# Optimization experiments

Hardware: AMD Instinct MI355X
Metric: run time of the kernel (lower is better)

## Reference

```python
import jax, jax.numpy as jnp
import numpy as np

R = 16            # search_range
D = 2 * R + 1     # 33 offsets per axis -> 1089 cost channels
B, C, H, W = 64, 256, 16, 16
OUT = 512         # conv channels for search_range=16
FULLY = 1024
EPS_BN = 1e-5
EPS_NORM = 1e-12
LRELU_SLOPE = 0.01


def l2_normalize(x):
    # torch F.normalize(x, dim=1, p=2): x / clamp_min(||x||_2, 1e-12)
    n = jnp.sqrt(jnp.sum(x * x, axis=1, keepdims=True))
    return x / jnp.maximum(n, EPS_NORM)


def cost_volume(c1, warp, r):
    # Fused equivalent of the original (2r+1)^2 Python-loop of slice/mul/mean:
    # one dense correlation GEMM over the padded map, then a gather of the
    # diagonal-band entries. cost[b,dy,dx,i,j] = mean_c c1[b,c,i,j]*pad[b,c,i+dy,j+dx]
    b, c, h, w = c1.shape
    d = 2 * r + 1
    padded = jnp.pad(warp, ((0, 0), (0, 0), (r, r), (r, r)))          # (B,C,h+2r,w+2r)
    full = jnp.einsum('bcij,bcuv->bijuv', c1, padded) / c             # (B,h,w,h+2r,w+2r)
    dy = jnp.arange(d)
    ii = jnp.arange(h)
    jj = jnp.arange(w)
    I = ii[None, None, :, None]                 # (1,1,h,1)
    J = jj[None, None, None, :]                 # (1,1,1,w)
    U = dy[:, None, None, None] + I             # (d,1,h,1)
    V = dy[None, :, None, None] + J             # (1,d,1,w)
    cost = full[:, I, J, U, V]                  # (B,d,d,h,w)
    cost = cost.reshape(b, d * d, h, w)
    return jnp.where(cost > 0, cost, LRELU_SLOPE * cost)  # LeakyReLU(0.01)


def conv_bn_relu(x, Wc, bc, g, be, stride):
    y = jax.lax.conv_general_dilated(
        x, Wc, window_strides=(stride, stride), padding=((1, 1), (1, 1)),
        dimension_numbers=('NCHW', 'OIHW', 'NCHW'))
    y = y + bc[None, :, None, None]
    # training-mode BatchNorm: biased batch stats over (B,H,W)
    mu = jnp.mean(y, axis=(0, 2, 3), keepdims=True)
    var = jnp.var(y, axis=(0, 2, 3), keepdims=True)
    y = (y - mu) * jax.lax.rsqrt(var + EPS_BN)
    y = y * g[None, :, None, None] + be[None, :, None, None]
    return jnp.maximum(y, 0.0)


def setup_inputs() -> dict:
    key = jax.random.key(0)
    ks = jax.random.split(key, 10)
    s = 0.02
    inp = {
        'feature1': jax.random.normal(ks[0], (B, C, H, W), jnp.float32),
        'feature2': jax.random.normal(ks[1], (B, C, H, W), jnp.float32),
        'W1': jax.random.normal(ks[2], (OUT, D * D, 3, 3), jnp.float32) * s,
        'b1': jnp.zeros((OUT,), jnp.float32),
        'g1': jnp.ones((OUT,), jnp.float32),
        'be1': jnp.zeros((OUT,), jnp.float32),
        'W2': jax.random.normal(ks[3], (OUT, OUT, 3, 3), jnp.float32) * s,
        'b2': jnp.zeros((OUT,), jnp.float32),
        'g2': jnp.ones((OUT,), jnp.float32),
        'be2': jnp.zeros((OUT,), jnp.float32),
        'W3': jax.random.normal(ks[4], (OUT, OUT, 3, 3), jnp.float32) * s,
        'b3': jnp.zeros((OUT,), jnp.float32),
        'g3': jnp.ones((OUT,), jnp.float32),
        'be3': jnp.zeros((OUT,), jnp.float32),
        'Wf1': jax.random.normal(ks[5], (FULLY, 256 * OUT), jnp.float32) * s,
        'bf1': jnp.zeros((FULLY,), jnp.float32),
        'Wf2': jax.random.normal(ks[6], (8, FULLY), jnp.float32) * s,
        'bf2': jnp.zeros((8,), jnp.float32),
    }
    return inp


def reference(feature1, feature2, W1, b1, g1, be1, W2, b2, g2, be2,
              W3, b3, g3, be3, Wf1, bf1, Wf2, bf2):
    # warped=False: normalize both feature maps
    gc = cost_volume(l2_normalize(feature1), l2_normalize(feature2), R)
    x = conv_bn_relu(gc, W1, b1, g1, be1, 1)
    x = conv_bn_relu(x, W2, b2, g2, be2, 1)
    x = conv_bn_relu(x, W3, b3, g3, be3, 1)
    x = x.reshape(x.shape[0], -1)               # (B, 512*16*16)
    x = jnp.maximum(x @ Wf1.T + bf1, 0.0)       # Linear + ReLU
    # Dropout treated as identity (deterministic reference)
    offset = x @ Wf2.T + bf2                    # (B, 8)
    return offset
```

## Files before the change

### kernel.cpp

```cpp
#include <hip/hip_runtime.h>
#include <hip/hip_bf16.h>
#include <stdint.h>


typedef unsigned short ushort_t;
typedef __attribute__((ext_vector_type(8))) short     bf16x8;
typedef __attribute__((ext_vector_type(8))) unsigned short u16x8;
typedef __attribute__((ext_vector_type(2))) unsigned short u16x2;
typedef __attribute__((ext_vector_type(4))) float     f32x4;

#define NB   64
#define NC   256
#define NP   256
#define KP1  1152
#define NOUT 512
#define NROWS 16384
#define KFC  131072
#define NF   1024
#define KSPL 32

__device__ __forceinline__ unsigned short f2bf(float x) {
  union { float f; unsigned u; } c; c.f = x;
  unsigned r = c.u + 0x7FFFu + ((c.u >> 16) & 1u);
  return (unsigned short)(r >> 16);
}
__device__ __forceinline__ float b2f(unsigned short u) {
  union { unsigned u; float f; } c; c.u = ((unsigned)u) << 16; return c.f;
}

__device__ __forceinline__ void gl_lds16(const void* g, void* l) {
  __builtin_amdgcn_global_load_lds(
      (const __attribute__((address_space(1))) unsigned int*)g,
      (__attribute__((address_space(3))) unsigned int*)l, 16, 0, 0);
}

__device__ __forceinline__ f32x4 mfma16(bf16x8 a, bf16x8 b, f32x4 c) {
  return __builtin_amdgcn_mfma_f32_16x16x32_bf16(a, b, c, 0, 0, 0);
}

__global__ __launch_bounds__(1024) void l2norm_t(
    const float* __restrict__ f1, const float* __restrict__ f2,
    ushort_t* __restrict__ AT, ushort_t* __restrict__ N2T)
{
  __shared__ float red[4][256];
  const float* src = blockIdx.y ? f2 : f1;
  ushort_t*    dst = blockIdx.y ? N2T : AT;
  const int b = blockIdx.x;
  const int pos = threadIdx.x & 255, q = threadIdx.x >> 8;
  const float* sb = src + (size_t)b * NC * NP;
  float v[64];
#pragma unroll
  for (int k = 0; k < 64; ++k) v[k] = sb[(q * 64 + k) * NP + pos];
  float sq = 0.f;
#pragma unroll
  for (int k = 0; k < 64; ++k) sq += v[k] * v[k];
  red[q][pos] = sq;
  __syncthreads();
  float tot = red[0][pos] + red[1][pos] + red[2][pos] + red[3][pos];
  float sc = 1.f / fmaxf(sqrtf(tot), 1e-12f);
  ushort_t* db = dst + ((size_t)b * NP + pos) * NC;
#pragma unroll
  for (int j = 0; j < 8; ++j) {
    u16x8 pk;
#pragma unroll
    for (int k = 0; k < 8; ++k) pk[k] = f2bf(v[j * 8 + k] * sc);
    *(u16x8*)(db + q * 64 + j * 8) = pk;
  }
}

#define T1P (9 * NOUT * KP1)
#define T23 (9 * NOUT * 512)
__global__ __launch_bounds__(256) void pack_all(
    const float* __restrict__ W1, const float* __restrict__ W2,
    const float* __restrict__ W3, ushort_t* __restrict__ Wp1,
    ushort_t* __restrict__ Wp2, ushort_t* __restrict__ Wp3)
{
  int p = blockIdx.x * 256 + threadIdx.x;
  const float* W; ushort_t* Wp; int Cin, Kp, q;
  if (p < T1P)            { W = W1; Wp = Wp1; Cin = 1089; Kp = KP1; q = p; }
  else if (p < T1P + T23) { W = W2; Wp = Wp2; Cin = 512;  Kp = 512; q = p - T1P; }
  else if (p < T1P + 2 * T23) { W = W3; Wp = Wp3; Cin = 512; Kp = 512; q = p - T1P - T23; }
  else return;
  int tap = q / (NOUT * Kp);
  int rem = q - tap * (NOUT * Kp);
  int o   = rem / Kp;
  int cin = rem - o * Kp;
  float v = (cin < Cin) ? W[((size_t)o * Cin + cin) * 9 + tap] : 0.f;
  Wp[q] = f2bf(v);
}

__global__ __launch_bounds__(256) void corr_gemm(
    const ushort_t* __restrict__ AT,
    const ushort_t* __restrict__ N2T,
    float* __restrict__ C)
{
  __shared__ ushort_t As[128 * 64];
  __shared__ ushort_t Bs[128 * 64];
  const int tid = threadIdx.x, lane = tid & 63, wave = tid >> 6;
  const int wr = wave >> 1, wc = wave & 1;
  const int la = lane & 15, lb = lane >> 4;
  const int b  = blockIdx.z;
  const int m0 = blockIdx.y * 128;
  const int n0 = blockIdx.x * 128;

  f32x4 acc[4][4];
#pragma unroll
  for (int i = 0; i < 4; ++i)
#pragma unroll
    for (int j = 0; j < 4; ++j) acc[i][j] = (f32x4){0.f, 0.f, 0.f, 0.f};

  const ushort_t* srcA[4];
  const ushort_t* srcB[4];
#pragma unroll
  for (int s = 0; s < 4; ++s) {
    int idx = tid + (s << 8);
    int row = idx >> 3, c16 = idx & 7;
    srcA[s] = AT  + ((size_t)b * NP + m0 + row) * NC + c16 * 8;
    srcB[s] = N2T + ((size_t)b * NP + n0 + row) * NC + c16 * 8;
  }

  for (int kc = 0; kc < NC; kc += 64) {
#pragma unroll
    for (int s = 0; s < 4; ++s) {
      int idx = tid + (s << 8);
      gl_lds16(srcA[s] + kc, &As[idx * 8]);
      gl_lds16(srcB[s] + kc, &Bs[idx * 8]);
    }
    __syncthreads();
#pragma unroll
    for (int kk = 0; kk < 2; ++kk) {
      bf16x8 af[4], bfv[4];
#pragma unroll
      for (int mi = 0; mi < 4; ++mi)
        af[mi] = *(const bf16x8*)&As[(wr * 64 + mi * 16 + la) * 64 + kk * 32 + lb * 8];
#pragma unroll
      for (int ni = 0; ni < 4; ++ni)
        bfv[ni] = *(const bf16x8*)&Bs[(wc * 64 + ni * 16 + la) * 64 + kk * 32 + lb * 8];
#pragma unroll
      for (int mi = 0; mi < 4; ++mi)
#pragma unroll
        for (int ni = 0; ni < 4; ++ni)
          acc[mi][ni] = mfma16(af[mi], bfv[ni], acc[mi][ni]);
    }
    __syncthreads();
  }

#pragma unroll
  for (int ni = 0; ni < 4; ++ni) {
    int col = n0 + wc * 64 + ni * 16 + la;
#pragma unroll
    for (int mi = 0; mi < 4; ++mi) {
      int p = m0 + wr * 64 + mi * 16 + lb * 4;
#pragma unroll
      for (int r = 0; r < 4; ++r)
        C[((size_t)b * NP + p + r) * NP + col] = acc[mi][ni][r];
    }
  }
}

__global__ __launch_bounds__(576) void cost_write(
    const float* __restrict__ C, ushort_t* __restrict__ costT)
{
  __shared__ float row[256];
  const int ij = blockIdx.x, b = blockIdx.y, tid = threadIdx.x;
  const float* cr = C + ((size_t)b * NP + ij) * NP;
  if (tid < 256) row[tid] = cr[tid];
  __syncthreads();
  const int i = ij >> 4, j = ij & 15;
  const int d0 = tid * 2;
  u16x2 pk;
#pragma unroll
  for (int q = 0; q < 2; ++q) {
    int dd = d0 + q;
    int dy = dd / 33;
    int dx = dd - dy * 33;
    int oi = dy + i - 16, oj = dx + j - 16;
    float v = 0.f;
    if (((unsigned)oi < 16u) & ((unsigned)oj < 16u))
      v = row[oi * 16 + oj] * (1.f / 256.f);
    v = v > 0.f ? v : 0.01f * v;
    pk[q] = f2bf(v);
  }
  *(u16x2*)(costT + ((size_t)b * NP + ij) * KP1 + d0) = pk;
}

__global__ __launch_bounds__(512, 1) void conv_fused(
    const ushort_t* __restrict__ X, const ushort_t* __restrict__ Wp,
    const float* __restrict__ bias, ushort_t* __restrict__ Y,
    float* __restrict__ st, const int K, const int TPT, const int NT,
    const ushort_t* __restrict__ zerot)
{
  __shared__ ushort_t lds[2 * 24576];
  const int tid = threadIdx.x;
  const int lane = tid & 63, wave = tid >> 6;
  const int wr = wave >> 2, wc = wave & 3;
  const int la = lane & 15, lb = lane >> 4;

  const int bid = blockIdx.x;
  const int L = ((bid & 7) << 5) + (bid >> 3);
  const int b = L >> 2;
  const int n0 = (L & 3) << 7;

  int amask[4];
  const ushort_t* abase[4];
  const ushort_t* bbase[2];
#pragma unroll
  for (int s = 0; s < 4; ++s) {
    int idx = tid + (s << 9);
    int ks = idx & 7, loc = (idx >> 3) & 63;
    int rA = ((s & 1) << 7) + ((s >> 1) << 6) + loc;
    int i = rA >> 4, j = rA & 15;
    int m = 0;
#pragma unroll
    for (int tap = 0; tap < 9; ++tap) {
      int i2 = i + tap / 3 - 1, j2 = j + tap % 3 - 1;
      if (((unsigned)i2 < 16u) & ((unsigned)j2 < 16u)) m |= 1 << tap;
    }
    amask[s] = m;
    abase[s] = X + (size_t)(b * NP + rA) * K + ((ks ^ (rA & 7)) << 3);
  }
#pragma unroll
  for (int s = 0; s < 2; ++s) {
    int idx = tid + (s << 9);
    int ks = idx & 7, loc = (idx >> 3) & 63;
    int rB = (s << 6) + loc;
    bbase[s] = Wp + (size_t)(n0 + rB) * K + ((ks ^ (rB & 7)) << 3);
  }

  const int ck0 = ((0 + lb) ^ (la & 7)) << 3;
  const int ck1 = ((4 + lb) ^ (la & 7)) << 3;
  const int a_base = wr * 4096 + la * 64;
  const int b_off  = 16384 + (wc * 32 + la) * 64;

  f32x4 acc[8][2];
#pragma unroll
  for (int i = 0; i < 8; ++i)
#pragma unroll
    for (int j = 0; j < 2; ++j) acc[i][j] = (f32x4){0.f, 0.f, 0.f, 0.f};

  auto tile_par = [&](int tg, int& toffA, size_t& wtap, int& tap) {
    tap = tg / TPT;
    int kc = (tg - tap * TPT) << 6;
    int ty = tap / 3;
    toffA = (ty * 16 + (tap - 3 * ty) - 17) * K + kc;
    wtap  = (size_t)tap * NOUT * K + kc;
  };

#define FSTAGE_A(S) { const ushort_t* gp = ((amask[S] >> tapN) & 1) ? abase[S] + toffN : zerot; \
                      gl_lds16(gp, &bufn[(tid + ((S) << 9)) * 8]); }
#define FSTAGE_B(S) gl_lds16(bbase[S] + wtapN, &bufn[16384 + (tid + ((S) << 9)) * 8]);
#define FREAD_A03() \
  Af[0][0] = *(const bf16x8*)&buf[a_base + 0    + ck0]; Af[0][1] = *(const bf16x8*)&buf[a_base + 0    + ck1]; \
  Af[1][0] = *(const bf16x8*)&buf[a_base + 1024 + ck0]; Af[1][1] = *(const bf16x8*)&buf[a_base + 1024 + ck1]; \
  Af[2][0] = *(const bf16x8*)&buf[a_base + 2048 + ck0]; Af[2][1] = *(const bf16x8*)&buf[a_base + 2048 + ck1]; \
  Af[3][0] = *(const bf16x8*)&buf[a_base + 3072 + ck0]; Af[3][1] = *(const bf16x8*)&buf[a_base + 3072 + ck1];
#define FREAD_A47() \
  Af[0][0] = *(const bf16x8*)&buf[a_base + 8192 + 0    + ck0]; Af[0][1] = *(const bf16x8*)&buf[a_base + 8192 + 0    + ck1]; \
  Af[1][0] = *(const bf16x8*)&buf[a_base + 8192 + 1024 + ck0]; Af[1][1] = *(const bf16x8*)&buf[a_base + 8192 + 1024 + ck1]; \
  Af[2][0] = *(const bf16x8*)&buf[a_base + 8192 + 2048 + ck0]; Af[2][1] = *(const bf16x8*)&buf[a_base + 8192 + 2048 + ck1]; \
  Af[3][0] = *(const bf16x8*)&buf[a_base + 8192 + 3072 + ck0]; Af[3][1] = *(const bf16x8*)&buf[a_base + 8192 + 3072 + ck1];
#define FREAD_B() \
  Bf[0][0] = *(const bf16x8*)&buf[b_off + 0    + ck0]; Bf[0][1] = *(const bf16x8*)&buf[b_off + 0    + ck1]; \
  Bf[1][0] = *(const bf16x8*)&buf[b_off + 1024 + ck0]; Bf[1][1] = *(const bf16x8*)&buf[b_off + 1024 + ck1];
#define FMFMA(AB) \
  acc[(AB)+0][0] = mfma16(Af[0][0], Bf[0][0], acc[(AB)+0][0]); \
  acc[(AB)+0][1] = mfma16(Af[0][0], Bf[1][0], acc[(AB)+0][1]); \
  acc[(AB)+1][0] = mfma16(Af[1][0], Bf[0][0], acc[(AB)+1][0]); \
  acc[(AB)+1][1] = mfma16(Af[1][0], Bf[1][0], acc[(AB)+1][1]); \
  acc[(AB)+2][0] = mfma16(Af[2][0], Bf[0][0], acc[(AB)+2][0]); \
  acc[(AB)+2][1] = mfma16(Af[2][0], Bf[1][0], acc[(AB)+2][1]); \
  acc[(AB)+3][0] = mfma16(Af[3][0], Bf[0][0], acc[(AB)+3][0]); \
  acc[(AB)+3][1] = mfma16(Af[3][0], Bf[1][0], acc[(AB)+3][1]); \
  acc[(AB)+0][0] = mfma16(Af[0][1], Bf[0][1], acc[(AB)+0][0]); \
  acc[(AB)+0][1] = mfma16(Af[0][1], Bf[1][1], acc[(AB)+0][1]); \
  acc[(AB)+1][0] = mfma16(Af[1][1], Bf[0][1], acc[(AB)+1][0]); \
  acc[(AB)+1][1] = mfma16(Af[1][1], Bf[1][1], acc[(AB)+1][1]); \
  acc[(AB)+2][0] = mfma16(Af[2][1], Bf[0][1], acc[(AB)+2][0]); \
  acc[(AB)+2][1] = mfma16(Af[2][1], Bf[1][1], acc[(AB)+2][1]); \
  acc[(AB)+3][0] = mfma16(Af[3][1], Bf[0][1], acc[(AB)+3][0]); \
  acc[(AB)+3][1] = mfma16(Af[3][1], Bf[1][1], acc[(AB)+3][1]);

  {
    ushort_t* bufn = &lds[0];
    int tapN, toffN; size_t wtapN;
    tile_par(0, toffN, wtapN, tapN);
    FSTAGE_A(0) FSTAGE_A(1) FSTAGE_B(0) FSTAGE_B(1) FSTAGE_A(2) FSTAGE_A(3)
  }
  asm volatile("s_waitcnt vmcnt(2)" ::: "memory");
  __builtin_amdgcn_s_barrier();

  for (int t = 0; t < NT - 1; ++t) {
    const ushort_t* buf = &lds[(t & 1) * 24576];
    ushort_t* bufn = &lds[((t + 1) & 1) * 24576];
    int tapN, toffN; size_t wtapN;
    tile_par(t + 1, toffN, wtapN, tapN);
    bf16x8 Af[4][2], Bf[2][2];

    FREAD_A03()
    FREAD_B()
    FSTAGE_A(0) FSTAGE_A(1) FSTAGE_B(0) FSTAGE_B(1)
    asm volatile("s_waitcnt vmcnt(4)" ::: "memory");
    __builtin_amdgcn_s_barrier();
    asm volatile("s_waitcnt lgkmcnt(0)" ::: "memory");
    __builtin_amdgcn_sched_barrier(0);
    __builtin_amdgcn_s_setprio(1);
    FMFMA(0)
    __builtin_amdgcn_s_setprio(0);

    FREAD_A47()
    FSTAGE_A(2) FSTAGE_A(3)
    asm volatile("s_waitcnt vmcnt(2)" ::: "memory");
    __builtin_amdgcn_s_barrier();
    asm volatile("s_waitcnt lgkmcnt(0)" ::: "memory");
    __builtin_amdgcn_sched_barrier(0);
    __builtin_amdgcn_s_setprio(1);
    FMFMA(4)
    __builtin_amdgcn_s_setprio(0);
  }

  {
    const ushort_t* buf = &lds[((NT - 1) & 1) * 24576];
    bf16x8 Af[4][2], Bf[2][2];
    FREAD_A03()
    FREAD_B()
    asm volatile("s_waitcnt vmcnt(0)" ::: "memory");
    __builtin_amdgcn_s_barrier();
    asm volatile("s_waitcnt lgkmcnt(0)" ::: "memory");
    __builtin_amdgcn_sched_barrier(0);
    FMFMA(0)
    FREAD_A47()
    asm volatile("s_waitcnt lgkmcnt(0)" ::: "memory");
    __builtin_amdgcn_sched_barrier(0);
    FMFMA(4)
  }

#pragma unroll
  for (int ni = 0; ni < 2; ++ni) {
    int col = n0 + wc * 32 + ni * 16 + la;
    float bv = bias[col];
    float s = 0.f, qq = 0.f;
#pragma unroll
    for (int mi = 0; mi < 8; ++mi) {
      int row = b * NP + wr * 128 + mi * 16 + lb * 4;
#pragma unroll
      for (int r = 0; r < 4; ++r) {
        float v = acc[mi][ni][r] + bv;
        Y[(size_t)(row + r) * NOUT + col] = f2bf(v);
        s += v; qq += v * v;
      }
    }
    s  += __shfl_xor(s, 16);  s  += __shfl_xor(s, 32);
    qq += __shfl_xor(qq, 16); qq += __shfl_xor(qq, 32);
    if (lb == 0) {
      atomicAdd(&st[col], s);
      atomicAdd(&st[512 + col], qq);
    }
  }
#undef FSTAGE_A
#undef FSTAGE_B
#undef FREAD_A03
#undef FREAD_A47
#undef FREAD_B
#undef FMFMA
}

__global__ __launch_bounds__(256) void bn_apply_s(
    const ushort_t* __restrict__ Y, const float* __restrict__ st,
    const float* __restrict__ g, const float* __restrict__ be,
    ushort_t* __restrict__ Xo)
{
  const size_t idx = (size_t)blockIdx.x * 256 + threadIdx.x;
  u16x8 a = *(const u16x8*)(Y + idx * 8);
  const int c0 = (int)((idx * 8) & 511);
  u16x8 pk;
#pragma unroll
  for (int q = 0; q < 8; ++q) {
    int cc = c0 + q;
    float y = b2f(a[q]);
    float mu  = st[cc] * (1.f / 16384.f);
    float var = st[512 + cc] * (1.f / 16384.f) - mu * mu;
    float s = rsqrtf(var + 1e-5f) * g[cc];
    pk[q] = f2bf(fmaxf((y - mu) * s + be[cc], 0.f));
  }
  *(u16x8*)(Xo + idx * 8) = pk;
}

__global__ __launch_bounds__(256) void bn_apply_ts(
    const ushort_t* __restrict__ Y, const float* __restrict__ st,
    const float* __restrict__ g, const float* __restrict__ be,
    ushort_t* __restrict__ Xf)
{
  __shared__ ushort_t T[64][65];
  const int c0  = blockIdx.x * 64;
  const int ij0 = blockIdx.y * 64;
  const int b   = blockIdx.z;
  const int tid = threadIdx.x;

#pragma unroll
  for (int it = 0; it < 16; ++it) {
    int e = it * 256 + tid;
    int ij = e >> 6, c = e & 63;
    int cg = c0 + c;
    float y = b2f(Y[((size_t)(b * NP + ij0 + ij)) * NOUT + cg]);
    float mu  = st[cg] * (1.f / 16384.f);
    float var = st[512 + cg] * (1.f / 16384.f) - mu * mu;
    float s = rsqrtf(var + 1e-5f) * g[cg];
    T[ij][c] = f2bf(fmaxf((y - mu) * s + be[cg], 0.f));
  }
  __syncthreads();
#pragma unroll
  for (int it = 0; it < 16; ++it) {
    int e = it * 256 + tid;
    int cr = e >> 6, ijc = e & 63;
    Xf[(size_t)b * KFC + (size_t)(c0 + cr) * NP + ij0 + ijc] = T[ijc][cr];
  }
}

__device__ __forceinline__ u16x8 pack8(float4 a, float4 b) {
  u16x8 r;
  r[0] = f2bf(a.x); r[1] = f2bf(a.y); r[2] = f2bf(a.z); r[3] = f2bf(a.w);
  r[4] = f2bf(b.x); r[5] = f2bf(b.y); r[6] = f2bf(b.z); r[7] = f2bf(b.w);
  return r;
}

__global__ __launch_bounds__(256) void fc1_gemm(
    const ushort_t* __restrict__ Xf, const float* __restrict__ Wf1,
    float* __restrict__ hacc)
{
  __shared__ ushort_t As[2][4096];
  __shared__ ushort_t Bs[2][4096];
  const int tid = threadIdx.x, lane = tid & 63, wave = tid >> 6;
  const int la = lane & 15, lb = lane >> 4;
  const int f0 = blockIdx.x * 64;
  const int k0 = blockIdx.y * 4096;

  f32x4 acc[4];
#pragma unroll
  for (int i = 0; i < 4; ++i) acc[i] = (f32x4){0.f, 0.f, 0.f, 0.f};

  const ushort_t* xrow0 = Xf + (size_t)(tid >> 3) * KFC + k0 + (tid & 7) * 8;
  const ushort_t* xrow1 = Xf + (size_t)((tid + 256) >> 3) * KFC + k0 + (tid & 7) * 8;
  const int brow = tid >> 2, kseg = (tid & 3) * 16;
  const float* wrow = Wf1 + (size_t)(f0 + brow) * KFC + k0 + kseg;
  const int bwr = brow * 64 + kseg;

  float4 w0, w1, w2, w3;

  gl_lds16(xrow0, &As[0][tid * 8]);
  gl_lds16(xrow1, &As[0][(tid + 256) * 8]);
  w0 = *(const float4*)(wrow + 0);
  w1 = *(const float4*)(wrow + 4);
  w2 = *(const float4*)(wrow + 8);
  w3 = *(const float4*)(wrow + 12);
  *(u16x8*)&Bs[0][bwr]     = pack8(w0, w1);
  *(u16x8*)&Bs[0][bwr + 8] = pack8(w2, w3);
  gl_lds16(xrow0 + 64, &As[1][tid * 8]);
  gl_lds16(xrow1 + 64, &As[1][(tid + 256) * 8]);
  w0 = *(const float4*)(wrow + 64);
  w1 = *(const float4*)(wrow + 68);
  w2 = *(const float4*)(wrow + 72);
  w3 = *(const float4*)(wrow + 76);
  asm volatile("s_waitcnt lgkmcnt(0)" ::: "memory");
  __builtin_amdgcn_s_barrier();

#define FC1_MFMA(CUR) \
  { \
    _Pragma("unroll") \
    for (int kk = 0; kk < 2; ++kk) { \
      bf16x8 bfv = *(const bf16x8*)&Bs[CUR][(wave * 16 + la) * 64 + kk * 32 + lb * 8]; \
      _Pragma("unroll") \
      for (int mi = 0; mi < 4; ++mi) { \
        bf16x8 av = *(const bf16x8*)&As[CUR][(mi * 16 + la) * 64 + kk * 32 + lb * 8]; \
        acc[mi] = mfma16(av, bfv, acc[mi]); \
      } \
    } \
  }

  for (int t = 0; t < 62; ++t) {
    const int cur = t & 1, nxt = cur ^ 1;
    FC1_MFMA(cur)
    *(u16x8*)&Bs[nxt][bwr]     = pack8(w0, w1);
    *(u16x8*)&Bs[nxt][bwr + 8] = pack8(w2, w3);
    {
      const float* wp = wrow + (t + 2) * 64;
      w0 = *(const float4*)(wp + 0);
      w1 = *(const float4*)(wp + 4);
      w2 = *(const float4*)(wp + 8);
      w3 = *(const float4*)(wp + 12);
    }
    asm volatile("s_waitcnt vmcnt(4)" ::: "memory");
    asm volatile("s_waitcnt lgkmcnt(0)" ::: "memory");
    __builtin_amdgcn_s_barrier();
    gl_lds16(xrow0 + (t + 2) * 64, &As[cur][tid * 8]);
    gl_lds16(xrow1 + (t + 2) * 64, &As[cur][(tid + 256) * 8]);
  }
  {
    FC1_MFMA(0)
    *(u16x8*)&Bs[1][bwr]     = pack8(w0, w1);
    *(u16x8*)&Bs[1][bwr + 8] = pack8(w2, w3);
    asm volatile("s_waitcnt vmcnt(0)" ::: "memory");
    asm volatile("s_waitcnt lgkmcnt(0)" ::: "memory");
    __builtin_amdgcn_s_barrier();
  }
  FC1_MFMA(1)
#undef FC1_MFMA

  float* slice = hacc + (size_t)blockIdx.y * NB * NF;
#pragma unroll
  for (int mi = 0; mi < 4; ++mi) {
    int row = mi * 16 + lb * 4;
#pragma unroll
    for (int r = 0; r < 4; ++r)
      slice[(size_t)(row + r) * NF + f0 + wave * 16 + la] = acc[mi][r];
  }
}

__global__ __launch_bounds__(256) void fc2_out(
    const float* __restrict__ hacc, const float* __restrict__ bf1,
    const float* __restrict__ Wf2, const float* __restrict__ bf2,
    float* __restrict__ out)
{
  const int b = blockIdx.x, tid = threadIdx.x;
  float a[8];
#pragma unroll
  for (int o = 0; o < 8; ++o) a[o] = 0.f;
  for (int f = tid; f < NF; f += 256) {
    float hv = bf1[f];
#pragma unroll 4
    for (int s = 0; s < KSPL; ++s)
      hv += hacc[((size_t)s * NB + b) * NF + f];
    hv = fmaxf(hv, 0.f);
#pragma unroll
    for (int o = 0; o < 8; ++o) a[o] += hv * Wf2[o * NF + f];
  }
  __shared__ float red[8][256];
#pragma unroll
  for (int o = 0; o < 8; ++o) red[o][tid] = a[o];
  __syncthreads();
  for (int s = 128; s > 0; s >>= 1) {
    if (tid < s) {
#pragma unroll
      for (int o = 0; o < 8; ++o) red[o][tid] += red[o][tid + s];
    }
    __syncthreads();
  }
  if (tid < 8) out[b * 8 + tid] = red[tid][0] + bf2[tid];
}

extern "C" void kernel_launch(void* const* d_in, const int* in_sizes, int n_in,
                              void* d_out, int out_size, void* d_ws, size_t ws_size,
                              hipStream_t stream) {
  const float* f1  = (const float*)d_in[0];
  const float* f2  = (const float*)d_in[1];
  const float* W1  = (const float*)d_in[2];
  const float* b1  = (const float*)d_in[3];
  const float* g1  = (const float*)d_in[4];
  const float* be1 = (const float*)d_in[5];
  const float* W2  = (const float*)d_in[6];
  const float* b2  = (const float*)d_in[7];
  const float* g2  = (const float*)d_in[8];
  const float* be2 = (const float*)d_in[9];
  const float* W3  = (const float*)d_in[10];
  const float* b3  = (const float*)d_in[11];
  const float* g3  = (const float*)d_in[12];
  const float* be3 = (const float*)d_in[13];
  const float* Wf1 = (const float*)d_in[14];
  const float* bf1 = (const float*)d_in[15];
  const float* Wf2 = (const float*)d_in[16];
  const float* bf2 = (const float*)d_in[17];
  float* out = (float*)d_out;

  char* ws = (char*)d_ws;
  size_t off = 0;
  auto alloc = [&](size_t bytes) -> void* {
    void* p = ws + off;
    off += (bytes + 255) & ~(size_t)255;
    return p;
  };

  ushort_t* zerot = (ushort_t*)alloc(256);
  float* st1  = (float*)alloc(1024 * 4);
  float* st2  = (float*)alloc(1024 * 4);
  float* st3  = (float*)alloc(1024 * 4);
  const size_t zero_bytes = off;

  float* hacc = (float*)alloc((size_t)KSPL * NB * NF * 4);
  const size_t SZ_AT   = (size_t)NB * NP * NC * 2;
  const size_t SZ_COST = (size_t)NB * NP * KP1 * 2;
  const size_t SZ_WP1  = (size_t)9 * NOUT * KP1 * 2;
  const size_t SZ_WP23 = (size_t)9 * NOUT * 512 * 2;
  ushort_t* AT    = (ushort_t*)alloc(SZ_AT);
  ushort_t* N2T   = (ushort_t*)alloc(SZ_AT);
  float*    Cbuf  = (float*)alloc((size_t)NB * NP * NP * 4);
  ushort_t* costT = (ushort_t*)alloc(SZ_COST);
  ushort_t* Wp1   = (ushort_t*)alloc(SZ_WP1);
  ushort_t* Wp2   = (ushort_t*)alloc(SZ_WP23);
  ushort_t* Wp3   = (ushort_t*)alloc(SZ_WP23);
  ushort_t* Ybuf  = (ushort_t*)alloc((size_t)NROWS * NOUT * 2);
  ushort_t* Xbuf  = (ushort_t*)alloc((size_t)NROWS * NOUT * 2);
  ushort_t* Xf    = (ushort_t*)alloc((size_t)NB * KFC * 2);

  hipMemsetAsync(ws, 0, zero_bytes, stream);

  l2norm_t<<<dim3(64, 2), 1024, 0, stream>>>(f1, f2, AT, N2T);

  pack_all<<<(T1P + 2 * T23 + 255) / 256, 256, 0, stream>>>(W1, W2, W3, Wp1, Wp2, Wp3);

  corr_gemm<<<dim3(2, 2, 64), 256, 0, stream>>>(AT, N2T, Cbuf);
  cost_write<<<dim3(256, 64), 576, 0, stream>>>(Cbuf, costT);

  conv_fused<<<256, 512, 0, stream>>>(costT, Wp1, b1, Ybuf, st1, KP1, 18, 162, zerot);
  bn_apply_s<<<4096, 256, 0, stream>>>(Ybuf, st1, g1, be1, Xbuf);

  conv_fused<<<256, 512, 0, stream>>>(Xbuf, Wp2, b2, Ybuf, st2, 512, 8, 72, zerot);
  bn_apply_s<<<4096, 256, 0, stream>>>(Ybuf, st2, g2, be2, Xbuf);

  conv_fused<<<256, 512, 0, stream>>>(Xbuf, Wp3, b3, Ybuf, st3, 512, 8, 72, zerot);
  bn_apply_ts<<<dim3(8, 4, 64), 256, 0, stream>>>(Ybuf, st3, g3, be3, Xf);

  fc1_gemm<<<dim3(16, KSPL), 256, 0, stream>>>(Xf, Wf1, hacc);
  fc2_out<<<64, 256, 0, stream>>>(hacc, bf1, Wf2, bf2, out);

  (void)in_sizes; (void)n_in; (void)out_size; (void)ws_size;
}
```

Measured before the change: 561.0 us.

## Halve conv M-tile to 128 rows and double grid for higher occupancy

New measurement: 593.2 us. 1.06x slower.

```diff
diff --git a/kernel.cpp b/kernel.cpp
--- a/kernel.cpp
+++ b/kernel.cpp
@@ -184,32 +184,33 @@
   *(u16x2*)(costT + ((size_t)b * NP + ij) * KP1 + d0) = pk;
 }
 
-__global__ __launch_bounds__(512, 1) void conv_fused(
+__global__ __launch_bounds__(512, 4) void conv_fused(
     const ushort_t* __restrict__ X, const ushort_t* __restrict__ Wp,
     const float* __restrict__ bias, ushort_t* __restrict__ Y,
     float* __restrict__ st, const int K, const int TPT, const int NT,
     const ushort_t* __restrict__ zerot)
 {
-  __shared__ ushort_t lds[2 * 24576];
+  __shared__ ushort_t lds[2 * 16384];
   const int tid = threadIdx.x;
   const int lane = tid & 63, wave = tid >> 6;
   const int wr = wave >> 2, wc = wave & 3;
   const int la = lane & 15, lb = lane >> 4;
 
   const int bid = blockIdx.x;
-  const int L = ((bid & 7) << 5) + (bid >> 3);
-  const int b = L >> 2;
+  const int L = ((bid & 7) << 6) + (bid >> 3);
+  const int b  = L >> 3;
+  const int mh = (L >> 2) & 1;
   const int n0 = (L & 3) << 7;
 
-  int amask[4];
-  const ushort_t* abase[4];
+  int amask[2];
+  const ushort_t* abase[2];
   const ushort_t* bbase[2];
 #pragma unroll
-  for (int s = 0; s < 4; ++s) {
+  for (int s = 0; s < 2; ++s) {
     int idx = tid + (s << 9);
-    int ks = idx & 7, loc = (idx >> 3) & 63;
-    int rA = ((s & 1) << 7) + ((s >> 1) << 6) + loc;
-    int i = rA >> 4, j = rA & 15;
+    int ks = idx & 7, row = idx >> 3;
+    int pos = mh * 128 + row;
+    int i = pos >> 4, j = pos & 15;
     int m = 0;
 #pragma unroll
     for (int tap = 0; tap < 9; ++tap) {
@@ -217,24 +218,20 @@
       if (((unsigned)i2 < 16u) & ((unsigned)j2 < 16u)) m |= 1 << tap;
     }
     amask[s] = m;
-    abase[s] = X + (size_t)(b * NP + rA) * K + ((ks ^ (rA & 7)) << 3);
-  }
-#pragma unroll
-  for (int s = 0; s < 2; ++s) {
-    int idx = tid + (s << 9);
-    int ks = idx & 7, loc = (idx >> 3) & 63;
-    int rB = (s << 6) + loc;
+    abase[s] = X + (size_t)(b * NP + pos) * K + ((ks ^ (row & 7)) << 3);
+    int rB = (s << 6) + row - (s << 6);
+    rB = row;
     bbase[s] = Wp + (size_t)(n0 + rB) * K + ((ks ^ (rB & 7)) << 3);
   }
 
   const int ck0 = ((0 + lb) ^ (la & 7)) << 3;
-  const int ck1 = ((4 + lb) ^ (la & 7)) << 3;
+  const int ck1 = (((4 + lb)) ^ (la & 7)) << 3;
   const int a_base = wr * 4096 + la * 64;
-  const int b_off  = 16384 + (wc * 32 + la) * 64;
-
-  f32x4 acc[8][2];
-#pragma unroll
-  for (int i = 0; i < 8; ++i)
+  const int b_off  = 8192 + (wc * 32 + la) * 64;
+
+  f32x4 acc[4][2];
+#pragma unroll
+  for (int i = 0; i < 4; ++i)
 #pragma unroll
     for (int j = 0; j < 2; ++j) acc[i][j] = (f32x4){0.f, 0.f, 0.f, 0.f};
 
@@ -248,17 +245,13 @@
 
 #define FSTAGE_A(S) { const ushort_t* gp = ((amask[S] >> tapN) & 1) ? abase[S] + toffN : zerot; \
                       gl_lds16(gp, &bufn[(tid + ((S) << 9)) * 8]); }
-#define FSTAGE_B(S) gl_lds16(bbase[S] + wtapN, &bufn[16384 + (tid + ((S) << 9)) * 8]);
-#define FREAD_A03() \
+#define FSTAGE_B(S) gl_lds16(bbase[S] + wtapN, &bufn[8192 + (tid + ((S) << 9)) * 8]);
+#define FREAD_A01() \
   Af[0][0] = *(const bf16x8*)&buf[a_base + 0    + ck0]; Af[0][1] = *(const bf16x8*)&buf[a_base + 0    + ck1]; \
-  Af[1][0] = *(const bf16x8*)&buf[a_base + 1024 + ck0]; Af[1][1] = *(const bf16x8*)&buf[a_base + 1024 + ck1]; \
-  Af[2][0] = *(const bf16x8*)&buf[a_base + 2048 + ck0]; Af[2][1] = *(const bf16x8*)&buf[a_base + 2048 + ck1]; \
-  Af[3][0] = *(const bf16x8*)&buf[a_base + 3072 + ck0]; Af[3][1] = *(const bf16x8*)&buf[a_base + 3072 + ck1];
-#define FREAD_A47() \
-  Af[0][0] = *(const bf16x8*)&buf[a_base + 8192 + 0    + ck0]; Af[0][1] = *(const bf16x8*)&buf[a_base + 8192 + 0    + ck1]; \
-  Af[1][0] = *(const bf16x8*)&buf[a_base + 8192 + 1024 + ck0]; Af[1][1] = *(const bf16x8*)&buf[a_base + 8192 + 1024 + ck1]; \
-  Af[2][0] = *(const bf16x8*)&buf[a_base + 8192 + 2048 + ck0]; Af[2][1] = *(const bf16x8*)&buf[a_base + 8192 + 2048 + ck1]; \
-  Af[3][0] = *(const bf16x8*)&buf[a_base + 8192 + 3072 + ck0]; Af[3][1] = *(const bf16x8*)&buf[a_base + 8192 + 3072 + ck1];
+  Af[1][0] = *(const bf16x8*)&buf[a_base + 1024 + ck0]; Af[1][1] = *(const bf16x8*)&buf[a_base + 1024 + ck1];
+#define FREAD_A23() \
+  Af[0][0] = *(const bf16x8*)&buf[a_base + 2048 + ck0]; Af[0][1] = *(const bf16x8*)&buf[a_base + 2048 + ck1]; \
+  Af[1][0] = *(const bf16x8*)&buf[a_base + 3072 + ck0]; Af[1][1] = *(const bf16x8*)&buf[a_base + 3072 + ck1];
 #define FREAD_B() \
   Bf[0][0] = *(const bf16x8*)&buf[b_off + 0    + ck0]; Bf[0][1] = *(const bf16x8*)&buf[b_off + 0    + ck1]; \
   Bf[1][0] = *(const bf16x8*)&buf[b_off + 1024 + ck0]; Bf[1][1] = *(const bf16x8*)&buf[b_off + 1024 + ck1];
@@ -267,39 +260,30 @@
   acc[(AB)+0][1] = mfma16(Af[0][0], Bf[1][0], acc[(AB)+0][1]); \
   acc[(AB)+1][0] = mfma16(Af[1][0], Bf[0][0], acc[(AB)+1][0]); \
   acc[(AB)+1][1] = mfma16(Af[1][0], Bf[1][0], acc[(AB)+1][1]); \
-  acc[(AB)+2][0] = mfma16(Af[2][0], Bf[0][0], acc[(AB)+2][0]); \
-  acc[(AB)+2][1] = mfma16(Af[2][0], Bf[1][0], acc[(AB)+2][1]); \
-  acc[(AB)+3][0] = mfma16(Af[3][0], Bf[0][0], acc[(AB)+3][0]); \
-  acc[(AB)+3][1] = mfma16(Af[3][0], Bf[1][0], acc[(AB)+3][1]); \
   acc[(AB)+0][0] = mfma16(Af[0][1], Bf[0][1], acc[(AB)+0][0]); \
   acc[(AB)+0][1] = mfma16(Af[0][1], Bf[1][1], acc[(AB)+0][1]); \
   acc[(AB)+1][0] = mfma16(Af[1][1], Bf[0][1], acc[(AB)+1][0]); \
-  acc[(AB)+1][1] = mfma16(Af[1][1], Bf[1][1], acc[(AB)+1][1]); \
-  acc[(AB)+2][0] = mfma16(Af[2][1], Bf[0][1], acc[(AB)+2][0]); \
-  acc[(AB)+2][1] = mfma16(Af[2][1], Bf[1][1], acc[(AB)+2][1]); \
-  acc[(AB)+3][0] = mfma16(Af[3][1], Bf[0][1], acc[(AB)+3][0]); \
-  acc[(AB)+3][1] = mfma16(Af[3][1], Bf[1][1], acc[(AB)+3][1]);
+  acc[(AB)+1][1] = mfma16(Af[1][1], Bf[1][1], acc[(AB)+1][1]);
 
   {
     ushort_t* bufn = &lds[0];
     int tapN, toffN; size_t wtapN;
     tile_par(0, toffN, wtapN, tapN);
-    FSTAGE_A(0) FSTAGE_A(1) FSTAGE_B(0) FSTAGE_B(1) FSTAGE_A(2) FSTAGE_A(3)
-  }
-  asm volatile("s_waitcnt vmcnt(2)" ::: "memory");
+    FSTAGE_A(0) FSTAGE_A(1) FSTAGE_B(0) FSTAGE_B(1)
+  }
+  asm volatile("s_waitcnt vmcnt(0)" ::: "memory");
   __builtin_amdgcn_s_barrier();
 
   for (int t = 0; t < NT - 1; ++t) {
-    const ushort_t* buf = &lds[(t & 1) * 24576];
-    ushort_t* bufn = &lds[((t + 1) & 1) * 24576];
+    const ushort_t* buf = &lds[(t & 1) * 16384];
+    ushort_t* bufn = &lds[((t + 1) & 1) * 16384];
     int tapN, toffN; size_t wtapN;
     tile_par(t + 1, toffN, wtapN, tapN);
-    bf16x8 Af[4][2], Bf[2][2];
-
-    FREAD_A03()
+    bf16x8 Af[2][2], Bf[2][2];
+
+    FREAD_A01()
     FREAD_B()
-    FSTAGE_A(0) FSTAGE_A(1) FSTAGE_B(0) FSTAGE_B(1)
-    asm volatile("s_waitcnt vmcnt(4)" ::: "memory");
+    FSTAGE_A(0) FSTAGE_A(1)
     __builtin_amdgcn_s_barrier();
     asm volatile("s_waitcnt lgkmcnt(0)" ::: "memory");
     __builtin_amdgcn_sched_barrier(0);
@@ -307,31 +291,30 @@
     FMFMA(0)
     __builtin_amdgcn_s_setprio(0);
 
-    FREAD_A47()
-    FSTAGE_A(2) FSTAGE_A(3)
-    asm volatile("s_waitcnt vmcnt(2)" ::: "memory");
+    FREAD_A23()
+    FSTAGE_B(0) FSTAGE_B(1)
+    asm volatile("s_waitcnt vmcnt(0)" ::: "memory");
     __builtin_amdgcn_s_barrier();
     asm volatile("s_waitcnt lgkmcnt(0)" ::: "memory");
     __builtin_amdgcn_sched_barrier(0);
     __builtin_amdgcn_s_setprio(1);
-    FMFMA(4)
+    FMFMA(2)
     __builtin_amdgcn_s_setprio(0);
+    __builtin_amdgcn_s_barrier();
   }
 
   {
-    const ushort_t* buf = &lds[((NT - 1) & 1) * 24576];
-    bf16x8 Af[4][2], Bf[2][2];
-    FREAD_A03()
+    const ushort_t* buf = &lds[((NT - 1) & 1) * 16384];
+    bf16x8 Af[2][2], Bf[2][2];
+    FREAD_A01()
     FREAD_B()
-    asm volatile("s_waitcnt vmcnt(0)" ::: "memory");
-    __builtin_amdgcn_s_barrier();
     asm volatile("s_waitcnt lgkmcnt(0)" ::: "memory");
     __builtin_amdgcn_sched_barrier(0);
     FMFMA(0)
-    FREAD_A47()
+    FREAD_A23()
     asm volatile("s_waitcnt lgkmcnt(0)" ::: "memory");
     __builtin_amdgcn_sched_barrier(0);
-    FMFMA(4)
+    FMFMA(2)
   }
 
 #pragma unroll
@@ -340,8 +323,8 @@
     float bv = bias[col];
     float s = 0.f, qq = 0.f;
 #pragma unroll
-    for (int mi = 0; mi < 8; ++mi) {
-      int row = b * NP + wr * 128 + mi * 16 + lb * 4;
+    for (int mi = 0; mi < 4; ++mi) {
+      int row = b * NP + mh * 128 + wr * 64 + mi * 16 + lb * 4;
 #pragma unroll
       for (int r = 0; r < 4; ++r) {
         float v = acc[mi][ni][r] + bv;
@@ -358,8 +341,8 @@
   }
 #undef FSTAGE_A
 #undef FSTAGE_B
-#undef FREAD_A03
-#undef FREAD_A47
+#undef FREAD_A01
+#undef FREAD_A23
 #undef FREAD_B
 #undef FMFMA
 }
@@ -609,13 +592,13 @@
   corr_gemm<<<dim3(2, 2, 64), 256, 0, stream>>>(AT, N2T, Cbuf);
   cost_write<<<dim3(256, 64), 576, 0, stream>>>(Cbuf, costT);
 
-  conv_fused<<<256, 512, 0, stream>>>(costT, Wp1, b1, Ybuf, st1, KP1, 18, 162, zerot);
+  conv_fused<<<512, 512, 0, stream>>>(costT, Wp1, b1, Ybuf, st1, KP1, 18, 162, zerot);
   bn_apply_s<<<4096, 256, 0, stream>>>(Ybuf, st1, g1, be1, Xbuf);
 
-  conv_fused<<<256, 512, 0, stream>>>(Xbuf, Wp2, b2, Ybuf, st2, 512, 8, 72, zerot);
+  conv_fused<<<512, 512, 0, stream>>>(Xbuf, Wp2, b2, Ybuf, st2, 512, 8, 72, zerot);
   bn_apply_s<<<4096, 256, 0, stream>>>(Ybuf, st2, g2, be2, Xbuf);
 
-  conv_fused<<<256, 512, 0, stream>>>(Xbuf, Wp3, b3, Ybuf, st3, 512, 8, 72, zerot);
+  conv_fused<<<512, 512, 0, stream>>>(Xbuf, Wp3, b3, Ybuf, st3, 512, 8, 72, zerot);
   bn_apply_ts<<<dim3(8, 4, 64), 256, 0, stream>>>(Ybuf, st3, g3, be3, Xf);
 
   fc1_gemm<<<dim3(16, KSPL), 256, 0, stream>>>(Xf, Wf1, hacc);
```
